# Kernel tuning notes

Measured on AMD Instinct MI355X. Metric: run time of the kernel, lower is better.

Reference implementation:

```python
import jax, jax.numpy as jnp
import numpy as np

N = 32768      # nodes
E = 524288     # edges (avg degree 16)
F = 64         # node_feat_dim
D = 64         # gnn_dim (= per-head out channels, concat=False)
ED = 32        # edge_feat_dim
L = 6          # num_layers
H = 2          # heads
C = D          # per-head channels
LN_EPS = 1e-5


def layer_norm(h, g, b):
    mu = jnp.mean(h, axis=-1, keepdims=True)
    var = jnp.mean((h - mu) ** 2, axis=-1, keepdims=True)
    return g * (h - mu) * jax.lax.rsqrt(var + LN_EPS) + b


def setup_inputs() -> dict:
    key = jax.random.key(0)
    ks = jax.random.split(key, 16)
    x = jax.random.normal(ks[0], (N, F), jnp.float32)
    edge_index = jax.random.randint(ks[1], (2, E), 0, N, jnp.int32)
    edge_attr = jax.random.normal(ks[2], (E, ED), jnp.float32)
    manual_gamma = 1.0 + 0.1 * jax.random.normal(ks[3], (L, D), jnp.float32)
    manual_beta = 0.1 * jax.random.normal(ks[4], (L, D), jnp.float32)
    # node_embed Linear(F, D)
    embed_W = jax.random.normal(ks[5], (F, D), jnp.float32) / np.float32(np.sqrt(F))
    embed_b = jnp.zeros((D,), jnp.float32)
    # per-layer LayerNorm affine params
    ln_gamma = jnp.ones((L, D), jnp.float32)
    ln_beta = jnp.zeros((L, D), jnp.float32)
    # per-layer GATConv params (shared lin for src/dst, PyG non-bipartite)
    lin_W = jax.random.normal(ks[6], (L, D, H * C), jnp.float32) / np.float32(np.sqrt(D))
    lin_edge_W = jax.random.normal(ks[7], (L, ED, H * C), jnp.float32) / np.float32(np.sqrt(ED))
    att_src = jax.random.normal(ks[8], (L, H, C), jnp.float32) / np.float32(np.sqrt(C))
    att_dst = jax.random.normal(ks[9], (L, H, C), jnp.float32) / np.float32(np.sqrt(C))
    att_edge = jax.random.normal(ks[10], (L, H, C), jnp.float32) / np.float32(np.sqrt(C))
    gat_bias = jnp.zeros((L, C), jnp.float32)
    # edge output head: Linear(2D+ED, D) -> ReLU -> Linear(D, 1)
    head_W1 = jax.random.normal(ks[11], (2 * D + ED, D), jnp.float32) / np.float32(np.sqrt(2 * D + ED))
    head_b1 = jnp.zeros((D,), jnp.float32)
    head_W2 = jax.random.normal(ks[12], (D, 1), jnp.float32) / np.float32(np.sqrt(D))
    head_b2 = jnp.zeros((1,), jnp.float32)
    return dict(x=x, edge_index=edge_index, edge_attr=edge_attr,
                manual_gamma=manual_gamma, manual_beta=manual_beta,
                embed_W=embed_W, embed_b=embed_b, ln_gamma=ln_gamma, ln_beta=ln_beta,
                lin_W=lin_W, lin_edge_W=lin_edge_W, att_src=att_src, att_dst=att_dst,
                att_edge=att_edge, gat_bias=gat_bias, head_W1=head_W1, head_b1=head_b1,
                head_W2=head_W2, head_b2=head_b2)


def reference(x, edge_index, edge_attr, manual_gamma, manual_beta,
              embed_W, embed_b, ln_gamma, ln_beta, lin_W, lin_edge_W,
              att_src, att_dst, att_edge, gat_bias, head_W1, head_b1,
              head_W2, head_b2):
    src, dst = edge_index[0], edge_index[1]
    # PyG GATConv default add_self_loops=True, fill_value='mean' for edge_attr
    loop = jnp.arange(N, dtype=edge_index.dtype)
    src_f = jnp.concatenate([src, loop])   # [E+N]
    dst_f = jnp.concatenate([dst, loop])
    deg = jax.ops.segment_sum(jnp.ones((E,), x.dtype), dst, num_segments=N)
    loop_attr = jax.ops.segment_sum(edge_attr, dst, num_segments=N) / jnp.maximum(deg, 1.0)[:, None]
    edge_attr_f = jnp.concatenate([edge_attr, loop_attr], axis=0)  # [E+N, ED]

    h = x @ embed_W + embed_b  # [N, D]
    for l in range(L):
        hn = layer_norm(h, ln_gamma[l], ln_beta[l])
        hm = manual_gamma[l][None, :] * hn + manual_beta[l][None, :]
        xh = (hm @ lin_W[l]).reshape(N, H, C)                      # [N,H,C]
        a_s = jnp.sum(xh * att_src[l][None], axis=-1)              # [N,H]
        a_d = jnp.sum(xh * att_dst[l][None], axis=-1)              # [N,H]
        eh = (edge_attr_f @ lin_edge_W[l]).reshape(-1, H, C)       # [E+N,H,C]
        a_e = jnp.sum(eh * att_edge[l][None], axis=-1)             # [E+N,H]
        alpha = jax.nn.leaky_relu(a_s[src_f] + a_d[dst_f] + a_e, 0.2)
        amax = jax.ops.segment_max(alpha, dst_f, num_segments=N)   # every node has a self-loop
        ex = jnp.exp(alpha - amax[dst_f])
        den = jax.ops.segment_sum(ex, dst_f, num_segments=N)
        w = ex / (den[dst_f] + 1e-16)                              # segment softmax [E+N,H]
        msg = xh[src_f] * w[..., None]                             # [E+N,H,C]
        out = jax.ops.segment_sum(msg, dst_f, num_segments=N)      # [N,H,C]
        h = jax.nn.relu(jnp.mean(out, axis=1) + gat_bias[l])       # concat=False -> head mean

    ef = jnp.concatenate([h[src], h[dst], edge_attr], axis=-1)     # [E, 2D+ED]
    hid = jax.nn.relu(ef @ head_W1 + head_b1)
    return (hid @ head_W2 + head_b2)[:, 0]                         # [E]
```

## Files before the change

### kernel.cpp

```cpp
#include <hip/hip_runtime.h>
#include <hip/hip_bf16.h>
#include <math.h>

#define NN 32768
#define EE 524288
#define LL 6

typedef __attribute__((ext_vector_type(8))) short short8;
typedef __attribute__((ext_vector_type(4))) float floatx4;

union U16x8 { short8 v; unsigned short u[8]; };

__device__ __forceinline__ unsigned short f2bf(float x) {
    union { float f; unsigned int u; } v; v.f = x;
    unsigned int r = v.u + 0x7fffu + ((v.u >> 16) & 1u);
    return (unsigned short)(r >> 16);
}
__device__ __forceinline__ float bf2f(unsigned short h) {
    union { unsigned int u; float f; } v; v.u = (unsigned int)h << 16;
    return v.f;
}


__global__ __launch_bounds__(1024) void scan_kernel(const int* __restrict__ deg,
                                                    int* __restrict__ row_ptr,
                                                    int* __restrict__ cnt) {
    __shared__ int bs[1024];
    int t = threadIdx.x;
    int base = t * 32;
    int loc[32];
    int s = 0;
#pragma unroll
    for (int i = 0; i < 32; ++i) { int v = deg[base + i]; loc[i] = s; s += v; }
    bs[t] = s;
    __syncthreads();
    for (int off = 1; off < 1024; off <<= 1) {
        int v = (t >= off) ? bs[t - off] : 0;
        __syncthreads();
        bs[t] += v;
        __syncthreads();
    }
    int pre = (t == 0) ? 0 : bs[t - 1];
#pragma unroll
    for (int i = 0; i < 32; ++i) { row_ptr[base + i] = pre + loc[i]; cnt[base + i] = 0; }
    if (t == 1023) row_ptr[NN] = bs[1023];
}

__global__ void fill_kernel(const int* __restrict__ src, const int* __restrict__ dst,
                            const int* __restrict__ row_ptr, int* __restrict__ cnt,
                            int2* __restrict__ sedge) {
    int e = blockIdx.x * 256 + threadIdx.x;
    if (e >= EE) return;
    int d = dst[e];
    int pos = row_ptr[d] + atomicAdd(&cnt[d], 1);
    sedge[pos] = make_int2(src[e], e);
}

__global__ __launch_bounds__(256) void smallprep_kernel(
    const float* __restrict__ lin_W, const float* __restrict__ head_W1,
    const float* __restrict__ lin_edge_W, const float* __restrict__ att_edge,
    const float* __restrict__ att_src, const float* __restrict__ att_dst,
    unsigned short* __restrict__ gBhi, unsigned short* __restrict__ gBlo,
    unsigned short* __restrict__ aeBhi, unsigned short* __restrict__ aeBlo,
    float* __restrict__ vs, float* __restrict__ vvd,
    unsigned short* __restrict__ w1chi, unsigned short* __restrict__ w1clo) {
    __shared__ float svb[384];
    int bb = blockIdx.x;
    int tid = threadIdx.x;
    if (bb < 7) {
        unsigned short* dh = gBhi + (size_t)bb * 128 * 64;
        unsigned short* dl = gBlo + (size_t)bb * 128 * 64;
        if (bb < 6) {
            int n2 = tid & 63, kh = tid >> 6;
            U16x8 hh[4], ll[4];
            for (int kk = 0; kk < 32; ++kk) {
                int j = kh * 32 + kk;
                int h = j >> 6, k = j & 63;
                float wv = 0.5f * lin_W[((size_t)bb * 64 + k) * 128 + h * 64 + n2];
                unsigned short h16 = f2bf(wv);
                hh[kk >> 3].u[kk & 7] = h16;
                ll[kk >> 3].u[kk & 7] = f2bf(wv - bf2f(h16));
            }
#pragma unroll
            for (int c = 0; c < 4; ++c) {
                int cg = kh * 4 + c;
                int off = n2 * 128 + ((cg ^ (n2 & 15)) << 3);
                *(short8*)(dh + off) = hh[c].v;
                *(short8*)(dl + off) = ll[c].v;
            }
        } else {
            int n = tid & 127, kh = tid >> 7;
            U16x8 hh[4], ll[4];
            for (int kk = 0; kk < 32; ++kk) {
                int k = kh * 32 + kk;
                float wv = (n < 64) ? head_W1[k * 64 + n] : head_W1[(64 + k) * 64 + (n - 64)];
                unsigned short h16 = f2bf(wv);
                hh[kk >> 3].u[kk & 7] = h16;
                ll[kk >> 3].u[kk & 7] = f2bf(wv - bf2f(h16));
            }
#pragma unroll
            for (int c = 0; c < 4; ++c) {
                int cg = kh * 4 + c;
                int off = n * 64 + ((cg ^ (n & 7)) << 3);
                *(short8*)(dh + off) = hh[c].v;
                *(short8*)(dl + off) = ll[c].v;
            }
        }
    } else if (bb == 7) {
        for (int t = tid; t < 384; t += 256) {
            int l = t / 64; int r = t & 63; int ed = r >> 1; int hh = r & 1;
            const float* w = lin_edge_W + l * 32 * 128 + ed * 128 + hh * 64;
            const float* a = att_edge + l * 128 + hh * 64;
            float s = 0.f;
#pragma unroll 8
            for (int c = 0; c < 64; ++c) s += w[c] * a[c];
            svb[t] = s;
        }
        int n = tid & 63, kc = tid >> 6;
#pragma unroll
        for (int j = 0; j < 8; ++j) {
            int k = kc * 8 + j;
            float wv = head_W1[(128 + k) * 64 + n];
            unsigned short h16 = f2bf(wv);
            w1chi[n * 32 + k] = h16;
            w1clo[n * 32 + k] = f2bf(wv - bf2f(h16));
        }
        __syncthreads();
        if (tid < 64) {
            int n2 = tid & 15, q = tid >> 4;
            U16x8 hi, lo;
#pragma unroll
            for (int i = 0; i < 8; ++i) {
                int k = q * 8 + i;
                float val = (n2 < 12) ? svb[(n2 >> 1) * 64 + k * 2 + (n2 & 1)] : 0.f;
                unsigned short h16 = f2bf(val);
                hi.u[i] = h16;
                lo.u[i] = f2bf(val - bf2f(h16));
            }
            *(short8*)(aeBhi + tid * 8) = hi.v;
            *(short8*)(aeBlo + tid * 8) = lo.v;
        }
    } else {
        int l = bb - 8;
        int sel = tid >> 7, idx = tid & 127;
        int h = idx >> 6, k = idx & 63;
        const float* att = (sel ? att_dst : att_src) + l * 128 + h * 64;
        const float* wr = lin_W + ((size_t)l * 64 + k) * 128 + h * 64;
        float s = 0.f;
#pragma unroll 8
        for (int c = 0; c < 64; ++c) s += wr[c] * att[c];
        (sel ? vvd : vs)[l * 128 + idx] = s;
    }
}

__global__ __launch_bounds__(256) void ae_deg_kernel(
    const float* __restrict__ edge_attr, const int* __restrict__ dst,
    const unsigned short* __restrict__ aeBhi, const unsigned short* __restrict__ aeBlo,
    float* __restrict__ aeo, unsigned short* __restrict__ eabf, int* __restrict__ deg) {
    __shared__ float tr[4][64 * 13];
    int tid = threadIdx.x;
    int w = tid >> 6, lane = tid & 63;
    int e0 = blockIdx.x * 256 + w * 64;
    int e = blockIdx.x * 256 + tid;
    atomicAdd(&deg[dst[e]], 1);
    short8 bhi = *(const short8*)(aeBhi + lane * 8);
    short8 blo = *(const short8*)(aeBlo + lane * 8);
    int r = lane & 15, q = lane >> 4;
    float* trw = tr[w];
#pragma unroll
    for (int t = 0; t < 4; ++t) {
        int er = e0 + t * 16 + r;
        const float4* p = (const float4*)(edge_attr + (size_t)er * 32 + q * 8);
        float4 f0 = p[0], f1 = p[1];
        float av[8] = {f0.x, f0.y, f0.z, f0.w, f1.x, f1.y, f1.z, f1.w};
        U16x8 hi, lo;
#pragma unroll
        for (int jj = 0; jj < 8; ++jj) {
            unsigned short h16 = f2bf(av[jj]);
            hi.u[jj] = h16;
            lo.u[jj] = f2bf(av[jj] - bf2f(h16));
        }
        *(short8*)(eabf + (size_t)er * 32 + q * 8) = hi.v;
        floatx4 acc = {};
        acc = __builtin_amdgcn_mfma_f32_16x16x32_bf16(lo.v, bhi, acc, 0, 0, 0);
        acc = __builtin_amdgcn_mfma_f32_16x16x32_bf16(hi.v, blo, acc, 0, 0, 0);
        acc = __builtin_amdgcn_mfma_f32_16x16x32_bf16(hi.v, bhi, acc, 0, 0, 0);
        if (r < 12) {
#pragma unroll
            for (int rr = 0; rr < 4; ++rr)
                trw[(t * 16 + q * 4 + rr) * 13 + r] = acc[rr];
        }
    }
#pragma unroll
    for (int l = 0; l < LL; ++l) {
        float2 v2;
        v2.x = trw[lane * 13 + l * 2];
        v2.y = trw[lane * 13 + l * 2 + 1];
        *(float2*)(aeo + (size_t)l * EE * 2 + (size_t)(e0 + lane) * 2) = v2;
    }
}

__global__ __launch_bounds__(256) void embed_ln_kernel(
    const float* __restrict__ x, const float* __restrict__ W, const float* __restrict__ b,
    const float* __restrict__ ln_g, const float* __restrict__ ln_b,
    const float* __restrict__ mg, const float* __restrict__ mb,
    const float* __restrict__ vs0, const float* __restrict__ vd0,
    unsigned short* __restrict__ hm_bf, float* __restrict__ a_s, float* __restrict__ a_d) {
    __shared__ float xr[4][64];
    int w = threadIdx.x >> 6, j = threadIdx.x & 63;
    int n = blockIdx.x * 4 + w;
    xr[w][j] = x[(size_t)n * 64 + j];
    __syncthreads();
    float acc = b[j];
#pragma unroll 8
    for (int k = 0; k < 64; ++k) acc += xr[w][k] * W[k * 64 + j];
    float s = acc, sq = acc * acc;
    for (int off = 1; off < 64; off <<= 1) { s += __shfl_xor(s, off); sq += __shfl_xor(sq, off); }
    float mu = s * (1.f / 64.f);
    float var = sq * (1.f / 64.f) - mu * mu;
    float rs = rsqrtf(var + 1e-5f);
    float hm = mg[j] * (ln_g[j] * (acc - mu) * rs + ln_b[j]) + mb[j];
    hm_bf[(size_t)n * 64 + j] = f2bf(hm);
    float s0 = hm * vs0[j], s1 = hm * vs0[64 + j];
    float d0 = hm * vd0[j], d1 = hm * vd0[64 + j];
    for (int off = 1; off < 64; off <<= 1) {
        s0 += __shfl_xor(s0, off); s1 += __shfl_xor(s1, off);
        d0 += __shfl_xor(d0, off); d1 += __shfl_xor(d1, off);
    }
    if (j == 0) {
        a_s[n * 2] = s0; a_s[n * 2 + 1] = s1;
        a_d[n * 2] = d0; a_d[n * 2 + 1] = d1;
    }
}

__device__ __forceinline__ void fma8h(uint4 pv, float w, float* a) {
    unsigned int u[4] = {pv.x, pv.y, pv.z, pv.w};
#pragma unroll
    for (int q = 0; q < 4; ++q) {
        union { unsigned int x; float f; } lo, hi;
        lo.x = u[q] << 16; hi.x = u[q] & 0xffff0000u;
        a[2 * q]     += w * lo.f;
        a[2 * q + 1] += w * hi.f;
    }
}

__global__ __launch_bounds__(256) void aggregate9_kernel(
    const unsigned short* __restrict__ hm_bf, const float* __restrict__ a_s,
    const float* __restrict__ a_d, const float* __restrict__ aeo,
    const int* __restrict__ row_ptr, const int2* __restrict__ sedge,
    unsigned short* __restrict__ Abf) {
    __shared__ float stg[4][4][64][4];
    int w = threadIdx.x >> 6, lane = threadIdx.x & 63;
    int g = lane >> 4, j = lane & 15;
    int ch = j & 7, hh = j >> 3;
    int n = blockIdx.x * 16 + w * 4 + g;
    const float2* as2 = (const float2*)a_s;
    const float2* ae2 = (const float2*)aeo;
    const uint4* hmv = (const uint4*)hm_bf;
    float2 adn = ((const float2*)a_d)[n];
    float2 asn = as2[n];
    uint4 pvself = hmv[(size_t)n * 8 + ch];
    int beg = row_ptr[n], end = row_ptr[n + 1];
    int degn = end - beg;

    float acc[8] = {};
    float den = 0.f, aex = 0.f, aey = 0.f;
    float* sg = &stg[w][g][0][0];

    for (int base = 0; base < degn; base += 64) {
        int cnt = degn - base; cnt = cnt > 64 ? 64 : cnt;
        int nchunk = (cnt + 15) >> 4;
        for (int it = 0; it < nchunk; ++it) {
            int s0 = it * 16;
            int rem = cnt - s0;
            float w0v = 0.f, w1v = 0.f;
            int sval = 0;
            if (j < rem) {
                int2 se = sedge[beg + base + s0 + j];
                float2 ae = ae2[se.y];
                float2 as = as2[se.x];
                aex += ae.x; aey += ae.y;
                float al0 = as.x + adn.x + ae.x; al0 = al0 > 0.f ? al0 : 0.2f * al0;
                float al1 = as.y + adn.y + ae.y; al1 = al1 > 0.f ? al1 : 0.2f * al1;
                w0v = __expf(al0);
                w1v = __expf(al1);
                sval = se.x;
            }
            float4 st;
            st.x = __int_as_float(sval); st.y = w0v; st.z = w1v; st.w = 0.f;
            *(float4*)(sg + (s0 + j) * 4) = st;
        }
        int c8 = (cnt + 7) & ~7;
        for (int s = 0; s < c8; s += 8) {
            float4 m[8];
#pragma unroll
            for (int u = 0; u < 8; ++u) m[u] = *(const float4*)(sg + (s + u) * 4);
            uint4 p[8];
#pragma unroll
            for (int u = 0; u < 8; ++u) p[u] = hmv[(size_t)__float_as_int(m[u].x) * 8 + ch];
#pragma unroll
            for (int u = 0; u < 8; ++u) {
                float b = hh ? m[u].z : m[u].y;
                den += b;
                fma8h(p[u], b, acc);
            }
        }
    }
#pragma unroll
    for (int m = 1; m < 16; m <<= 1) {
        aex += __shfl_xor(aex, m);
        aey += __shfl_xor(aey, m);
    }
    float invd = 1.f / fmaxf((float)degn, 1.f);
    float al0 = asn.x + adn.x + aex * invd; al0 = al0 > 0.f ? al0 : 0.2f * al0;
    float al1 = asn.y + adn.y + aey * invd; al1 = al1 > 0.f ? al1 : 0.2f * al1;
    float ws = hh ? __expf(al1) : __expf(al0);
    den += ws;
    fma8h(pvself, ws, acc);
    float inv = 1.f / (den + 1e-16f);
    U16x8 hb;
#pragma unroll
    for (int q = 0; q < 8; ++q) hb.u[q] = f2bf(acc[q] * inv);
    int cg = hh * 8 + ch;
    *(short8*)(Abf + (size_t)n * 128 + ((cg ^ (n & 15)) << 3)) = hb.v;
}

__global__ __launch_bounds__(256) void post_gemm(
    const unsigned short* __restrict__ Abf, const unsigned short* __restrict__ gBhi,
    const unsigned short* __restrict__ gBlo, const float* __restrict__ bias,
    const float* __restrict__ ln_g, const float* __restrict__ ln_b,
    const float* __restrict__ mg, const float* __restrict__ mb,
    const float* __restrict__ vsn, const float* __restrict__ vdn,
    unsigned short* __restrict__ hm_bf, float* __restrict__ a_s, float* __restrict__ a_d) {
    __shared__ unsigned short Ahi[64 * 128];
    __shared__ unsigned short Bhi[64 * 128], Blo[64 * 128];
    int tid = threadIdx.x;
    {
        const uint4* sa = (const uint4*)(Abf + (size_t)blockIdx.x * 64 * 128);
        const uint4* sh = (const uint4*)gBhi;
        const uint4* sl = (const uint4*)gBlo;
        for (int i = tid; i < 1024; i += 256) {
            ((uint4*)Ahi)[i] = sa[i];
            ((uint4*)Bhi)[i] = sh[i];
            ((uint4*)Blo)[i] = sl[i];
        }
    }
    __syncthreads();

    int w = tid >> 6, lane = tid & 63, col = lane & 15, quad = lane >> 4;
    int m = w * 16 + col;
    floatx4 acc[4] = {};
#pragma unroll
    for (int s = 0; s < 4; ++s) {
        int ca = (quad + 4 * s) ^ col;
        short8 ahi = *(const short8*)(Ahi + m * 128 + ca * 8);
#pragma unroll
        for (int t = 0; t < 4; ++t) {
            int off = (t * 16 + col) * 128 + ca * 8;
            short8 bhi = *(const short8*)(Bhi + off);
            short8 blo = *(const short8*)(Blo + off);
            acc[t] = __builtin_amdgcn_mfma_f32_16x16x32_bf16(ahi, blo, acc[t], 0, 0, 0);
            acc[t] = __builtin_amdgcn_mfma_f32_16x16x32_bf16(ahi, bhi, acc[t], 0, 0, 0);
        }
    }
    int nodebase = blockIdx.x * 64 + w * 16;
    float bv[4];
#pragma unroll
    for (int t = 0; t < 4; ++t) bv[t] = bias[t * 16 + col];
    float vsv[4], vsv1[4], vdv[4], vdv1[4], lg[4], lb[4], mgv[4], mbv[4];
#pragma unroll
    for (int t = 0; t < 4; ++t) {
        int c = t * 16 + col;
        vsv[t] = vsn[c]; vsv1[t] = vsn[64 + c];
        vdv[t] = vdn[c]; vdv1[t] = vdn[64 + c];
        lg[t] = ln_g[c]; lb[t] = ln_b[c];
        mgv[t] = mg[c]; mbv[t] = mb[c];
    }
#pragma unroll
    for (int r = 0; r < 4; ++r) {
        int node = nodebase + quad * 4 + r;
        float hv[4];
        float s = 0.f, sq = 0.f;
#pragma unroll
        for (int t = 0; t < 4; ++t) {
            float v = acc[t][r] + bv[t];
            v = v > 0.f ? v : 0.f;
            hv[t] = v;
            s += v; sq += v * v;
        }
        for (int off = 1; off < 16; off <<= 1) { s += __shfl_xor(s, off); sq += __shfl_xor(sq, off); }
        float mu = s * (1.f / 64.f);
        float var = sq * (1.f / 64.f) - mu * mu;
        float rs = rsqrtf(var + 1e-5f);
        float s0 = 0.f, s1 = 0.f, d0 = 0.f, d1 = 0.f;
#pragma unroll
        for (int t = 0; t < 4; ++t) {
            float hmv = mgv[t] * (lg[t] * (hv[t] - mu) * rs + lb[t]) + mbv[t];
            hm_bf[(size_t)node * 64 + t * 16 + col] = f2bf(hmv);
            s0 += hmv * vsv[t]; s1 += hmv * vsv1[t];
            d0 += hmv * vdv[t]; d1 += hmv * vdv1[t];
        }
        for (int off = 1; off < 16; off <<= 1) {
            s0 += __shfl_xor(s0, off); s1 += __shfl_xor(s1, off);
            d0 += __shfl_xor(d0, off); d1 += __shfl_xor(d1, off);
        }
        if (col == 0) {
            a_s[node * 2] = s0; a_s[node * 2 + 1] = s1;
            a_d[node * 2] = d0; a_d[node * 2 + 1] = d1;
        }
    }
}

__global__ __launch_bounds__(256) void postuv_gemm(
    const unsigned short* __restrict__ Abf, const unsigned short* __restrict__ gB5hi,
    const unsigned short* __restrict__ gB5lo, const float* __restrict__ bias,
    const unsigned short* __restrict__ gB6hi, const unsigned short* __restrict__ gB6lo,
    unsigned short* __restrict__ uv) {
    __shared__ unsigned short lds[24576];
    unsigned short* Ahi  = lds;
    unsigned short* B5hi = lds + 8192;
    unsigned short* B5lo = lds + 16384;
    unsigned short* A2hi = lds;
    unsigned short* A2lo = lds + 4096;
    unsigned short* B6hi = lds + 8192;
    unsigned short* B6lo = lds + 16384;
    int tid = threadIdx.x;
    {
        const uint4* sa = (const uint4*)(Abf + (size_t)blockIdx.x * 64 * 128);
        const uint4* sh = (const uint4*)gB5hi;
        const uint4* sl = (const uint4*)gB5lo;
        for (int i = tid; i < 1024; i += 256) {
            ((uint4*)Ahi)[i] = sa[i];
            ((uint4*)B5hi)[i] = sh[i];
            ((uint4*)B5lo)[i] = sl[i];
        }
    }
    __syncthreads();

    int w = tid >> 6, lane = tid & 63, col = lane & 15, quad = lane >> 4;
    int m = w * 16 + col;
    floatx4 acc[4] = {};
#pragma unroll
    for (int s = 0; s < 4; ++s) {
        int ca = (quad + 4 * s) ^ col;
        short8 ahi = *(const short8*)(Ahi + m * 128 + ca * 8);
#pragma unroll
        for (int t = 0; t < 4; ++t) {
            int off = (t * 16 + col) * 128 + ca * 8;
            short8 bhi = *(const short8*)(B5hi + off);
            short8 blo = *(const short8*)(B5lo + off);
            acc[t] = __builtin_amdgcn_mfma_f32_16x16x32_bf16(ahi, blo, acc[t], 0, 0, 0);
            acc[t] = __builtin_amdgcn_mfma_f32_16x16x32_bf16(ahi, bhi, acc[t], 0, 0, 0);
        }
    }
    float bv[4];
#pragma unroll
    for (int t = 0; t < 4; ++t) bv[t] = bias[t * 16 + col];
    __syncthreads();
#pragma unroll
    for (int t = 0; t < 4; ++t) {
        int c = t * 16 + col;
        int cg = c >> 3, cr = c & 7;
#pragma unroll
        for (int r = 0; r < 4; ++r) {
            float v = acc[t][r] + bv[t];
            v = v > 0.f ? v : 0.f;
            int i = w * 16 + quad * 4 + r;
            int off = i * 64 + ((cg ^ (i & 7)) << 3) + cr;
            unsigned short hh = f2bf(v);
            A2hi[off] = hh;
            A2lo[off] = f2bf(v - bf2f(hh));
        }
    }
    for (int i = tid; i < 1024; i += 256) {
        ((uint4*)B6hi)[i] = ((const uint4*)gB6hi)[i];
        ((uint4*)B6lo)[i] = ((const uint4*)gB6lo)[i];
    }
    __syncthreads();

    floatx4 acc2[8] = {};
#pragma unroll
    for (int s = 0; s < 2; ++s) {
        int ca = (quad + 4 * s) ^ (col & 7);
        short8 a2h = *(const short8*)(A2hi + m * 64 + ca * 8);
        short8 a2l = *(const short8*)(A2lo + m * 64 + ca * 8);
#pragma unroll
        for (int t = 0; t < 8; ++t) {
            int off = (t * 16 + col) * 64 + ca * 8;
            short8 bh = *(const short8*)(B6hi + off);
            short8 bl = *(const short8*)(B6lo + off);
            acc2[t] = __builtin_amdgcn_mfma_f32_16x16x32_bf16(a2l, bh, acc2[t], 0, 0, 0);
            acc2[t] = __builtin_amdgcn_mfma_f32_16x16x32_bf16(a2h, bl, acc2[t], 0, 0, 0);
            acc2[t] = __builtin_amdgcn_mfma_f32_16x16x32_bf16(a2h, bh, acc2[t], 0, 0, 0);
        }
    }
    int nodebase = blockIdx.x * 64 + w * 16;
#pragma unroll
    for (int t = 0; t < 8; ++t)
#pragma unroll
        for (int r = 0; r < 4; ++r)
            uv[(size_t)(nodebase + quad * 4 + r) * 128 + t * 16 + col] = f2bf(acc2[t][r]);
}

__global__ __launch_bounds__(256) void head2_kernel(
    const unsigned short* __restrict__ uv, const int* __restrict__ src,
    const int* __restrict__ dst, const unsigned short* __restrict__ eabf,
    const unsigned short* __restrict__ w1chi, const unsigned short* __restrict__ w1clo,
    const float* __restrict__ b1, const float* __restrict__ W2,
    const float* __restrict__ b2, float* __restrict__ out) {
    __shared__ float g[64][68];
    __shared__ unsigned short Abf[64 * 40];
    __shared__ unsigned short Bh[64 * 40], Bl[64 * 40];
    __shared__ int sA[64], dA[64];
    int tid = threadIdx.x;
    int base = blockIdx.x * 64;
    if (tid < 64) sA[tid] = src[base + tid];
    else if (tid < 128) dA[tid - 64] = dst[base + tid - 64];
    {
        int n = tid >> 2, c = tid & 3;
        *(short8*)(Bh + n * 40 + c * 8) = *(const short8*)(w1chi + n * 32 + c * 8);
        *(short8*)(Bl + n * 40 + c * 8) = *(const short8*)(w1clo + n * 32 + c * 8);
    }
    {
        int e = tid >> 2, q = tid & 3;
        *(short8*)(Abf + e * 40 + q * 8) = *(const short8*)(eabf + (size_t)(base + e) * 32 + q * 8);
    }
    __syncthreads();
    {
        int e = tid >> 2, q = tid & 3;
        const uint4* su = (const uint4*)(uv + (size_t)sA[e] * 128);
        const uint4* dv = (const uint4*)(uv + (size_t)dA[e] * 128);
        uint4 U0 = su[2 * q], U1 = su[2 * q + 1];
        uint4 V0 = dv[8 + 2 * q], V1 = dv[9 + 2 * q];
        const float4* b1p = (const float4*)(b1 + q * 16);
        float bb[16];
#pragma unroll
        for (int j = 0; j < 4; ++j) {
            float4 b4 = b1p[j];
            bb[4 * j] = b4.x; bb[4 * j + 1] = b4.y; bb[4 * j + 2] = b4.z; bb[4 * j + 3] = b4.w;
        }
        unsigned int uw[8] = {U0.x, U0.y, U0.z, U0.w, U1.x, U1.y, U1.z, U1.w};
        unsigned int vw[8] = {V0.x, V0.y, V0.z, V0.w, V1.x, V1.y, V1.z, V1.w};
        float* gr = &g[e][q * 16];
#pragma unroll
        for (int j = 0; j < 8; ++j) {
            gr[2 * j] = bf2f((unsigned short)(uw[j] & 0xffff)) +
                        bf2f((unsigned short)(vw[j] & 0xffff)) + bb[2 * j];
            gr[2 * j + 1] = bf2f((unsigned short)(uw[j] >> 16)) +
                            bf2f((unsigned short)(vw[j] >> 16)) + bb[2 * j + 1];
        }
    }
    __syncthreads();

    int lane = tid & 63, w = tid >> 6, col = lane & 15, quad = lane >> 4;
    short8 a = *(const short8*)(Abf + (w * 16 + col) * 40 + quad * 8);
    floatx4 acc[4] = {};
#pragma unroll
    for (int t = 0; t < 4; ++t) {
        int off = (t * 16 + col) * 40 + quad * 8;
        short8 bh = *(const short8*)(Bh + off);
        short8 bl = *(const short8*)(Bl + off);
        acc[t] = __builtin_amdgcn_mfma_f32_16x16x32_bf16(a, bl, acc[t], 0, 0, 0);
        acc[t] = __builtin_amdgcn_mfma_f32_16x16x32_bf16(a, bh, acc[t], 0, 0, 0);
    }
    float sv[4] = {0.f, 0.f, 0.f, 0.f};
#pragma unroll
    for (int t = 0; t < 4; ++t) {
        float w2v = W2[t * 16 + col];
#pragma unroll
        for (int r = 0; r < 4; ++r) {
            float hid = acc[t][r] + g[w * 16 + quad * 4 + r][t * 16 + col];
            hid = hid > 0.f ? hid : 0.f;
            sv[r] += hid * w2v;
        }
    }
    float b2v = b2[0];
#pragma unroll
    for (int r = 0; r < 4; ++r) {
        float v = sv[r];
        v += __shfl_xor(v, 1);
        v += __shfl_xor(v, 2);
        v += __shfl_xor(v, 4);
        v += __shfl_xor(v, 8);
        if (col == 0) out[base + w * 16 + quad * 4 + r] = v + b2v;
    }
}


extern "C" void kernel_launch(void* const* d_in, const int* in_sizes, int n_in,
                              void* d_out, int out_size, void* d_ws, size_t ws_size,
                              hipStream_t stream) {
    const float* x            = (const float*)d_in[0];
    const int*   edge_index   = (const int*)d_in[1];
    const float* edge_attr    = (const float*)d_in[2];
    const float* manual_gamma = (const float*)d_in[3];
    const float* manual_beta  = (const float*)d_in[4];
    const float* embed_W      = (const float*)d_in[5];
    const float* embed_b      = (const float*)d_in[6];
    const float* ln_gamma     = (const float*)d_in[7];
    const float* ln_beta      = (const float*)d_in[8];
    const float* lin_W        = (const float*)d_in[9];
    const float* lin_edge_W   = (const float*)d_in[10];
    const float* att_src      = (const float*)d_in[11];
    const float* att_dst      = (const float*)d_in[12];
    const float* att_edge     = (const float*)d_in[13];
    const float* gat_bias     = (const float*)d_in[14];
    const float* head_W1      = (const float*)d_in[15];
    const float* head_b1      = (const float*)d_in[16];
    const float* head_W2      = (const float*)d_in[17];
    const float* head_b2      = (const float*)d_in[18];
    float* out = (float*)d_out;

    const int* src = edge_index;
    const int* dst = edge_index + EE;

    char* ws = (char*)d_ws;
    size_t off = 0;
    auto alloc = [&](size_t bytes) {
        void* p = ws + off;
        off += (bytes + 255) & ~(size_t)255;
        return p;
    };
    int*   deg        = (int*)alloc(NN * 4);
    int*   row_ptr    = (int*)alloc((NN + 1) * 4);
    int*   cnt        = (int*)alloc(NN * 4);
    int2*  sedge      = (int2*)alloc((size_t)EE * 8);
    float* aeo        = (float*)alloc((size_t)LL * EE * 2 * 4);
    float* vs         = (float*)alloc(LL * 128 * 4);
    float* vvd        = (float*)alloc(LL * 128 * 4);
    float* a_s        = (float*)alloc((size_t)NN * 2 * 4);
    float* a_d        = (float*)alloc((size_t)NN * 2 * 4);
    unsigned short* Abf   = (unsigned short*)alloc((size_t)NN * 128 * 2);
    unsigned short* hm_bf = (unsigned short*)alloc((size_t)NN * 64 * 2);
    unsigned short* uvbuf = (unsigned short*)alloc((size_t)NN * 128 * 2);
    unsigned short* eabf  = (unsigned short*)alloc((size_t)EE * 32 * 2);
    unsigned short* gBhi  = (unsigned short*)alloc((size_t)7 * 128 * 64 * 2);
    unsigned short* gBlo  = (unsigned short*)alloc((size_t)7 * 128 * 64 * 2);
    unsigned short* w1chi = (unsigned short*)alloc(64 * 32 * 2);
    unsigned short* w1clo = (unsigned short*)alloc(64 * 32 * 2);
    unsigned short* aeBhi = (unsigned short*)alloc(64 * 8 * 2);
    unsigned short* aeBlo = (unsigned short*)alloc(64 * 8 * 2);
    if (off > ws_size) return;

    hipMemsetAsync(deg, 0, NN * 4, stream);

    smallprep_kernel<<<14, 256, 0, stream>>>(lin_W, head_W1, lin_edge_W, att_edge,
                                             att_src, att_dst, gBhi, gBlo, aeBhi, aeBlo,
                                             vs, vvd, w1chi, w1clo);
    ae_deg_kernel<<<EE / 256, 256, 0, stream>>>(edge_attr, dst, aeBhi, aeBlo, aeo, eabf, deg);
    scan_kernel<<<1, 1024, 0, stream>>>(deg, row_ptr, cnt);
    fill_kernel<<<EE / 256, 256, 0, stream>>>(src, dst, row_ptr, cnt, sedge);
    embed_ln_kernel<<<NN / 4, 256, 0, stream>>>(x, embed_W, embed_b, ln_gamma, ln_beta,
                                                manual_gamma, manual_beta, vs, vvd,
                                                hm_bf, a_s, a_d);

    for (int l = 0; l < LL; ++l) {
        aggregate9_kernel<<<NN / 16, 256, 0, stream>>>(
            hm_bf, a_s, a_d, aeo + (size_t)l * EE * 2, row_ptr, sedge, Abf);
        if (l < LL - 1) {
            post_gemm<<<NN / 64, 256, 0, stream>>>(
                Abf, gBhi + (size_t)l * 128 * 64, gBlo + (size_t)l * 128 * 64,
                gat_bias + l * 64, ln_gamma + (l + 1) * 64, ln_beta + (l + 1) * 64,
                manual_gamma + (l + 1) * 64, manual_beta + (l + 1) * 64,
                vs + (l + 1) * 128, vvd + (l + 1) * 128, hm_bf, a_s, a_d);
        } else {
            postuv_gemm<<<NN / 64, 256, 0, stream>>>(
                Abf, gBhi + (size_t)l * 128 * 64, gBlo + (size_t)l * 128 * 64,
                gat_bias + l * 64, gBhi + (size_t)6 * 128 * 64,
                gBlo + (size_t)6 * 128 * 64, uvbuf);
        }
    }

    head2_kernel<<<EE / 64, 256, 0, stream>>>(uvbuf, src, dst, eabf, w1chi, w1clo,
                                              head_b1, head_W2, head_b2, out);
}
```

Baseline: 457.6 us.

## Pack per-edge src and all-layer edge attention into CSR-ordered 64B records

The fill kernel now writes, at each CSR position, a 64-byte record holding the source index and the edge attention logits for all six layers. The aggregation kernel reads src and its layer's logit from that contiguous record instead of doing an indirect gather into a per-layer array through the edge id. It also folds the degree memset into the smallprep kernel and adds nontemporal loads and stores on streaming buffers. This trades a larger one-time scatter write in fill, and more bytes per edge, for sequential per-layer reads in the six aggregation passes.

Measured after the change: 456.5 us. About the same (-0.2%).

```diff
diff --git a/kernel.cpp b/kernel.cpp
--- a/kernel.cpp
+++ b/kernel.cpp
@@ -8,6 +8,8 @@
 
 typedef __attribute__((ext_vector_type(8))) short short8;
 typedef __attribute__((ext_vector_type(4))) float floatx4;
+typedef __attribute__((ext_vector_type(4))) float fx4;
+typedef __attribute__((ext_vector_type(4))) unsigned int ux4;
 
 union U16x8 { short8 v; unsigned short u[8]; };
 
@@ -47,13 +49,21 @@
 }
 
 __global__ void fill_kernel(const int* __restrict__ src, const int* __restrict__ dst,
-                            const int* __restrict__ row_ptr, int* __restrict__ cnt,
-                            int2* __restrict__ sedge) {
+                            const float* __restrict__ aeo, const int* __restrict__ row_ptr,
+                            int* __restrict__ cnt, float* __restrict__ aeP) {
     int e = blockIdx.x * 256 + threadIdx.x;
     if (e >= EE) return;
     int d = dst[e];
     int pos = row_ptr[d] + atomicAdd(&cnt[d], 1);
-    sedge[pos] = make_int2(src[e], e);
+    const float2* ae2 = (const float2*)aeo;
+    float2 a0 = ae2[e],          a1 = ae2[EE + e],     a2 = ae2[2 * EE + e];
+    float2 a3 = ae2[3 * EE + e], a4 = ae2[4 * EE + e], a5 = ae2[5 * EE + e];
+    fx4 r0 = {__int_as_float(src[e]), 0.f, a0.x, a0.y};
+    fx4 r1 = {a1.x, a1.y, a2.x, a2.y};
+    fx4 r2 = {a3.x, a3.y, a4.x, a4.y};
+    fx4 r3 = {a5.x, a5.y, 0.f, 0.f};
+    fx4* R = (fx4*)(aeP + (size_t)pos * 16);
+    R[0] = r0; R[1] = r1; R[2] = r2; R[3] = r3;
 }
 
 __global__ __launch_bounds__(256) void smallprep_kernel(
@@ -63,7 +73,8 @@
     unsigned short* __restrict__ gBhi, unsigned short* __restrict__ gBlo,
     unsigned short* __restrict__ aeBhi, unsigned short* __restrict__ aeBlo,
     float* __restrict__ vs, float* __restrict__ vvd,
-    unsigned short* __restrict__ w1chi, unsigned short* __restrict__ w1clo) {
+    unsigned short* __restrict__ w1chi, unsigned short* __restrict__ w1clo,
+    int* __restrict__ deg) {
     __shared__ float svb[384];
     int bb = blockIdx.x;
     int tid = threadIdx.x;
@@ -140,7 +151,7 @@
             *(short8*)(aeBhi + tid * 8) = hi.v;
             *(short8*)(aeBlo + tid * 8) = lo.v;
         }
-    } else {
+    } else if (bb < 14) {
         int l = bb - 8;
         int sel = tid >> 7, idx = tid & 127;
         int h = idx >> 6, k = idx & 63;
@@ -150,6 +161,9 @@
 #pragma unroll 8
         for (int c = 0; c < 64; ++c) s += wr[c] * att[c];
         (sel ? vvd : vs)[l * 128 + idx] = s;
+    } else {
+        int i = (bb - 14) * 1024 + tid * 4;
+        *(int4*)(deg + i) = make_int4(0, 0, 0, 0);
     }
 }
 
@@ -170,8 +184,9 @@
 #pragma unroll
     for (int t = 0; t < 4; ++t) {
         int er = e0 + t * 16 + r;
-        const float4* p = (const float4*)(edge_attr + (size_t)er * 32 + q * 8);
-        float4 f0 = p[0], f1 = p[1];
+        const fx4* p = (const fx4*)(edge_attr + (size_t)er * 32 + q * 8);
+        fx4 f0 = __builtin_nontemporal_load(p);
+        fx4 f1 = __builtin_nontemporal_load(p + 1);
         float av[8] = {f0.x, f0.y, f0.z, f0.w, f1.x, f1.y, f1.z, f1.w};
         U16x8 hi, lo;
 #pragma unroll
@@ -180,7 +195,7 @@
             hi.u[jj] = h16;
             lo.u[jj] = f2bf(av[jj] - bf2f(h16));
         }
-        *(short8*)(eabf + (size_t)er * 32 + q * 8) = hi.v;
+        __builtin_nontemporal_store(hi.v, (short8*)(eabf + (size_t)er * 32 + q * 8));
         floatx4 acc = {};
         acc = __builtin_amdgcn_mfma_f32_16x16x32_bf16(lo.v, bhi, acc, 0, 0, 0);
         acc = __builtin_amdgcn_mfma_f32_16x16x32_bf16(hi.v, blo, acc, 0, 0, 0);
@@ -244,18 +259,16 @@
     }
 }
 
-__global__ __launch_bounds__(256) void aggregate9_kernel(
+__global__ __launch_bounds__(256) void aggregate10_kernel(
     const unsigned short* __restrict__ hm_bf, const float* __restrict__ a_s,
-    const float* __restrict__ a_d, const float* __restrict__ aeo,
-    const int* __restrict__ row_ptr, const int2* __restrict__ sedge,
-    unsigned short* __restrict__ Abf) {
+    const float* __restrict__ a_d, const float* __restrict__ aeP,
+    const int* __restrict__ row_ptr, unsigned short* __restrict__ Abf, int aeoff) {
     __shared__ float stg[4][4][64][4];
     int w = threadIdx.x >> 6, lane = threadIdx.x & 63;
     int g = lane >> 4, j = lane & 15;
     int ch = j & 7, hh = j >> 3;
     int n = blockIdx.x * 16 + w * 4 + g;
     const float2* as2 = (const float2*)a_s;
-    const float2* ae2 = (const float2*)aeo;
     const uint4* hmv = (const uint4*)hm_bf;
     float2 adn = ((const float2*)a_d)[n];
     float2 asn = as2[n];
@@ -276,15 +289,16 @@
             float w0v = 0.f, w1v = 0.f;
             int sval = 0;
             if (j < rem) {
-                int2 se = sedge[beg + base + s0 + j];
-                float2 ae = ae2[se.y];
-                float2 as = as2[se.x];
+                const char* rec = (const char*)aeP + ((size_t)(beg + base + s0 + j) << 6);
+                int sv = *(const int*)rec;
+                float2 ae = *(const float2*)(rec + aeoff);
+                float2 as = as2[sv];
                 aex += ae.x; aey += ae.y;
                 float al0 = as.x + adn.x + ae.x; al0 = al0 > 0.f ? al0 : 0.2f * al0;
                 float al1 = as.y + adn.y + ae.y; al1 = al1 > 0.f ? al1 : 0.2f * al1;
                 w0v = __expf(al0);
                 w1v = __expf(al1);
-                sval = se.x;
+                sval = sv;
             }
             float4 st;
             st.x = __int_as_float(sval); st.y = w0v; st.z = w1v; st.w = 0.f;
@@ -322,7 +336,7 @@
 #pragma unroll
     for (int q = 0; q < 8; ++q) hb.u[q] = f2bf(acc[q] * inv);
     int cg = hh * 8 + ch;
-    *(short8*)(Abf + (size_t)n * 128 + ((cg ^ (n & 15)) << 3)) = hb.v;
+    __builtin_nontemporal_store(hb.v, (short8*)(Abf + (size_t)n * 128 + ((cg ^ (n & 15)) << 3)));
 }
 
 __global__ __launch_bounds__(256) void post_gemm(
@@ -336,11 +350,11 @@
     __shared__ unsigned short Bhi[64 * 128], Blo[64 * 128];
     int tid = threadIdx.x;
     {
-        const uint4* sa = (const uint4*)(Abf + (size_t)blockIdx.x * 64 * 128);
+        const ux4* sa = (const ux4*)(Abf + (size_t)blockIdx.x * 64 * 128);
         const uint4* sh = (const uint4*)gBhi;
         const uint4* sl = (const uint4*)gBlo;
         for (int i = tid; i < 1024; i += 256) {
-            ((uint4*)Ahi)[i] = sa[i];
+            ((ux4*)Ahi)[i] = __builtin_nontemporal_load(sa + i);
             ((uint4*)Bhi)[i] = sh[i];
             ((uint4*)Blo)[i] = sl[i];
         }
@@ -426,11 +440,11 @@
     unsigned short* B6lo = lds + 16384;
     int tid = threadIdx.x;
     {
-        const uint4* sa = (const uint4*)(Abf + (size_t)blockIdx.x * 64 * 128);
+        const ux4* sa = (const ux4*)(Abf + (size_t)blockIdx.x * 64 * 128);
         const uint4* sh = (const uint4*)gB5hi;
         const uint4* sl = (const uint4*)gB5lo;
         for (int i = tid; i < 1024; i += 256) {
-            ((uint4*)Ahi)[i] = sa[i];
+            ((ux4*)Ahi)[i] = __builtin_nontemporal_load(sa + i);
             ((uint4*)B5hi)[i] = sh[i];
             ((uint4*)B5lo)[i] = sl[i];
         }
@@ -523,7 +537,9 @@
     }
     {
         int e = tid >> 2, q = tid & 3;
-        *(short8*)(Abf + e * 40 + q * 8) = *(const short8*)(eabf + (size_t)(base + e) * 32 + q * 8);
+        short8 v = __builtin_nontemporal_load(
+            (const short8*)(eabf + (size_t)(base + e) * 32 + q * 8));
+        *(short8*)(Abf + e * 40 + q * 8) = v;
     }
     __syncthreads();
     {
@@ -624,7 +640,7 @@
     int*   deg        = (int*)alloc(NN * 4);
     int*   row_ptr    = (int*)alloc((NN + 1) * 4);
     int*   cnt        = (int*)alloc(NN * 4);
-    int2*  sedge      = (int2*)alloc((size_t)EE * 8);
+    float* aeP        = (float*)alloc((size_t)EE * 64);
     float* aeo        = (float*)alloc((size_t)LL * EE * 2 * 4);
     float* vs         = (float*)alloc(LL * 128 * 4);
     float* vvd        = (float*)alloc(LL * 128 * 4);
@@ -642,21 +658,19 @@
     unsigned short* aeBlo = (unsigned short*)alloc(64 * 8 * 2);
     if (off > ws_size) return;
 
-    hipMemsetAsync(deg, 0, NN * 4, stream);
-
-    smallprep_kernel<<<14, 256, 0, stream>>>(lin_W, head_W1, lin_edge_W, att_edge,
+    smallprep_kernel<<<46, 256, 0, stream>>>(lin_W, head_W1, lin_edge_W, att_edge,
                                              att_src, att_dst, gBhi, gBlo, aeBhi, aeBlo,
-                                             vs, vvd, w1chi, w1clo);
+                                             vs, vvd, w1chi, w1clo, deg);
     ae_deg_kernel<<<EE / 256, 256, 0, stream>>>(edge_attr, dst, aeBhi, aeBlo, aeo, eabf, deg);
     scan_kernel<<<1, 1024, 0, stream>>>(deg, row_ptr, cnt);
-    fill_kernel<<<EE / 256, 256, 0, stream>>>(src, dst, row_ptr, cnt, sedge);
+    fill_kernel<<<EE / 256, 256, 0, stream>>>(src, dst, aeo, row_ptr, cnt, aeP);
     embed_ln_kernel<<<NN / 4, 256, 0, stream>>>(x, embed_W, embed_b, ln_gamma, ln_beta,
                                                 manual_gamma, manual_beta, vs, vvd,
                                                 hm_bf, a_s, a_d);
 
     for (int l = 0; l < LL; ++l) {
-        aggregate9_kernel<<<NN / 16, 256, 0, stream>>>(
-            hm_bf, a_s, a_d, aeo + (size_t)l * EE * 2, row_ptr, sedge, Abf);
+        aggregate10_kernel<<<NN / 16, 256, 0, stream>>>(
+            hm_bf, a_s, a_d, aeP, row_ptr, Abf, 8 + 8 * l);
         if (l < LL - 1) {
             post_gemm<<<NN / 64, 256, 0, stream>>>(
                 Abf, gBhi + (size_t)l * 128 * 64, gBlo + (size_t)l * 128 * 64,
```
